# Optimization experiments

Hardware: AMD Instinct MI355X
Metric: run time of the kernel (lower is better)

The kernel has to match this reference:

```python
import jax, jax.numpy as jnp
import numpy as np

N_NODES = 50000
N_EDGES = 800000
HIDDEN = 128
OUT = 128


def setup_inputs() -> dict:
    key = jax.random.key(0)
    k1, k2, k3, k4, k5, k6 = jax.random.split(key, 6)
    h = jax.random.normal(k1, (N_NODES, HIDDEN), dtype=jnp.float32)
    src = jax.random.randint(k2, (N_EDGES,), 0, N_NODES, dtype=jnp.int64)
    dst = jax.random.randint(k3, (N_EDGES,), 0, N_NODES, dtype=jnp.int64)
    scale = 1.0 / np.sqrt(HIDDEN)
    W_edge = jax.random.normal(k4, (OUT, HIDDEN), dtype=jnp.float32) * scale
    W_self = jax.random.normal(k5, (OUT, HIDDEN), dtype=jnp.float32) * scale
    b_self = jax.random.normal(k6, (OUT,), dtype=jnp.float32) * scale
    return {"h": h, "src": src, "dst": dst, "W_edge": W_edge, "W_self": W_self, "b_self": b_self}


def reference(h, src, dst, W_edge, W_self, b_self):
    n = h.shape[0]
    # edge_transform(src_features): same linear on every edge -> transform nodes once, then gather
    msg_node = h @ W_edge.T                       # [N, OUT]
    msg = msg_node[src]                           # [E, OUT] gather
    sums = jax.ops.segment_sum(msg, dst, num_segments=n)  # [N, OUT] scatter-add
    deg = jax.ops.segment_sum(jnp.ones((dst.shape[0],), dtype=h.dtype), dst, num_segments=n)
    h1 = sums / jnp.maximum(deg, 1.0)[:, None]    # mean; zero in-degree -> 0 (DGL semantics)
    out = jax.nn.relu(h @ W_self.T + b_self + h1)
    return out
```

## Files before the change

kernel.cpp:

```cpp
#include <hip/hip_runtime.h>

#define N_HID 128
#define CAP   32
#define OVF_CAP 8192
#define NSLICE 8
#define PBLK   256

typedef short bf16x8 __attribute__((ext_vector_type(8)));
typedef float f32x4  __attribute__((ext_vector_type(4)));

static __device__ __forceinline__ unsigned short f2bf(float f)
{
    unsigned int u = __float_as_uint(f);
    u = (u + 0x7fffu + ((u >> 16) & 1u)) >> 16;
    return (unsigned short)u;
}
static __device__ __forceinline__ unsigned int pack2(float a, float b)
{
    return (unsigned int)f2bf(a) | ((unsigned int)f2bf(b) << 16);
}
static __device__ __forceinline__ float bf2f(unsigned int bits16)
{
    return __uint_as_float(bits16 << 16);
}
static __device__ __forceinline__ int slice_of(int d, float sln)
{
    int sl = (int)((float)d * sln);
    return sl > NSLICE - 1 ? NSLICE - 1 : sl;
}

__global__ __launch_bounds__(256) void count_fragw_cast(
    const int* __restrict__ dst, int* __restrict__ blockCnt,
    int* __restrict__ cnt, int* __restrict__ ovfn, int E, int n, float sln,
    const float* __restrict__ We, const float* __restrict__ Ws,
    unsigned short* __restrict__ Be, unsigned short* __restrict__ Bs,
    const float* __restrict__ h, unsigned short* __restrict__ hbf, int total)
{
    int t = threadIdx.x, b = blockIdx.x;

    if (b >= PBLK + 16) {
        int idx = (b - PBLK - 16) * 2048 + t * 8;
        if (idx + 8 <= total) {
            float4 v0 = *(const float4*)&h[idx];
            float4 v1 = *(const float4*)&h[idx + 4];
            uint4 pk;
            pk.x = pack2(v0.x, v0.y);
            pk.y = pack2(v0.z, v0.w);
            pk.z = pack2(v1.x, v1.y);
            pk.w = pack2(v1.z, v1.w);
            *(uint4*)&hbf[idx] = pk;
        }
        return;
    }

    if (b >= PBLK) {
        int bb = b - PBLK;
        const float* srcw = (bb < 8) ? We : Ws;
        unsigned short* dstF = (bb < 8) ? Be : Bs;
        int rt = bb & 7;
        int kc = t >> 6, l = t & 63, m = l & 15, q = l >> 4;
        const float* p = &srcw[(size_t)(rt * 16 + m) * N_HID + kc * 32 + q * 8];
        float4 v0 = *(const float4*)p;
        float4 v1 = *(const float4*)(p + 4);
        uint4 pk;
        pk.x = pack2(v0.x, v0.y);
        pk.y = pack2(v0.z, v0.w);
        pk.z = pack2(v1.x, v1.y);
        pk.w = pack2(v1.z, v1.w);
        *(uint4*)&dstF[(size_t)rt * 2048 + kc * 512 + l * 8] = pk;
        return;
    }

    for (int i = b * 256 + t; i < n; i += PBLK * 256) cnt[i] = 0;
    if (b == 0 && t == 0) *ovfn = 0;

    int c[NSLICE];
#pragma unroll
    for (int s = 0; s < NSLICE; ++s) c[s] = 0;

    for (int e = b * 256 + t; e < E; e += PBLK * 256) {
        int sl = slice_of(dst[e], sln);
#pragma unroll
        for (int s = 0; s < NSLICE; ++s) c[s] += (sl == s);
    }

    __shared__ int red[NSLICE * 4];
    int lane = t & 63, wid = t >> 6;
#pragma unroll
    for (int s = 0; s < NSLICE; ++s) {
        int v = c[s];
#pragma unroll
        for (int off = 32; off; off >>= 1) v += __shfl_down(v, off);
        if (lane == 0) red[s * 4 + wid] = v;
    }
    __syncthreads();
    if (t < NSLICE)
        blockCnt[t * PBLK + b] = red[t*4+0] + red[t*4+1] + red[t*4+2] + red[t*4+3];
}

__global__ __launch_bounds__(256) void part_scan(
    const int* __restrict__ blockCnt, int* __restrict__ blockBase,
    int* __restrict__ sbase, int E)
{
    __shared__ int wsm[4];
    int t = threadIdx.x, lane = t & 63, wid = t >> 6;
    int v[8]; int s = 0;
#pragma unroll
    for (int i = 0; i < 8; ++i) { v[i] = blockCnt[t * 8 + i]; s += v[i]; }
    int val = s;
#pragma unroll
    for (int off = 1; off < 64; off <<= 1) {
        int y = __shfl_up(val, off);
        if (lane >= off) val += y;
    }
    if (lane == 63) wsm[wid] = val;
    __syncthreads();
    if (t == 0) { int a = 0; for (int w = 0; w < 4; ++w) { int tmp = wsm[w]; wsm[w] = a; a += tmp; } }
    __syncthreads();
    int excl = wsm[wid] + val - s;
#pragma unroll
    for (int i = 0; i < 8; ++i) { int tv = v[i]; blockBase[t * 8 + i] = excl; excl += tv; }
    __syncthreads();
    if (t < NSLICE) sbase[t] = blockBase[t * PBLK];
    if (t == 0)     sbase[NSLICE] = E;
}

__global__ __launch_bounds__(256) void part_scatter(
    const int* __restrict__ src, const int* __restrict__ dst,
    const int* __restrict__ blockBase, unsigned int* __restrict__ part,
    int E, int n, float sln)
{
    __shared__ int cur[NSLICE];
    int t = threadIdx.x, b = blockIdx.x;
    if (t < NSLICE) cur[t] = blockBase[t * PBLK + b];
    __syncthreads();
    for (int e = b * 256 + t; e < E; e += PBLK * 256) {
        int d = dst[e], s = src[e];
        int sl  = slice_of(d, sln);
        int pos = atomicAdd(&cur[sl], 1);
        part[pos] = ((unsigned int)d << 16) | (unsigned int)s;
    }
}

__global__ __launch_bounds__(256) void bucket_scatter2(
    const unsigned int* __restrict__ part,
    const int* __restrict__ sbase,
    int* __restrict__ cnt,
    unsigned short* __restrict__ bucket,
    int* __restrict__ ovfn,
    long long* __restrict__ ovf)
{
    const int slice = blockIdx.x & 7;
    const int g     = blockIdx.x >> 3;
    const int nG    = (int)(gridDim.x >> 3);
    const int lo    = sbase[slice];
    const int hi    = sbase[slice + 1];
    const int m     = hi - lo;

    const int chunk = (m + nG - 1) / nG;
    const int e0 = lo + g * chunk;
    int e1 = e0 + chunk; if (e1 > hi) e1 = hi;

    for (int e = e0 + (int)threadIdx.x; e < e1; e += 256) {
        unsigned int pk = part[e];
        int d = (int)(pk >> 16);
        int s = (int)(pk & 0xffffu);
        int c = atomicAdd(&cnt[d], 1);
        if (c < CAP) {
            bucket[(size_t)d * CAP + c] = (unsigned short)s;
        } else {
            int o = atomicAdd(ovfn, 1);
            if (o < OVF_CAP) ovf[o] = ((long long)d << 32) | (unsigned int)s;
        }
    }
}

__global__ __launch_bounds__(256) void gather_gemm(
    const int* __restrict__ cnt,
    const unsigned short* __restrict__ bucket,
    const int* __restrict__ ovfn,
    const long long* __restrict__ ovf,
    const unsigned short* __restrict__ hbf,
    const unsigned short* __restrict__ Be,
    const unsigned short* __restrict__ Bsf,
    const float* __restrict__ bias,
    float* __restrict__ out,
    int n, int nrt)
{
    __shared__ __align__(16) unsigned int wl[16 * 68];

    const int t    = threadIdx.x;
    const int wid  = t >> 6;
    const int lane = t & 63;
    const int q    = lane >> 4;
    const int s    = lane & 15;
    const int slice = blockIdx.x & 7;
    const int g     = blockIdx.x >> 3;
    const int tLo = (int)(((long long)slice * nrt) >> 3);
    const int tHi = (int)(((long long)(slice + 1) * nrt) >> 3);
    const int tile = tLo + g;
    if (tile >= tHi) return;

    const uint4* h4 = (const uint4*)hbf;
    const unsigned int* h32 = (const unsigned int*)hbf;

    const int nodeBase = tile * 16 + wid * 4;
    int cntv = cnt[tile * 16 + s];
    unsigned int bkv = ((const unsigned int*)bucket)[(size_t)nodeBase * 16 + lane];

#pragma unroll
    for (int k = 0; k < 4; ++k) {
        const int mm   = wid * 4 + k;
        const int node = tile * 16 + mm;
        float a0=0.f,a1=0.f,a2=0.f,a3=0.f,a4=0.f,a5=0.f,a6=0.f,a7=0.f;
        int deg = 0;
        if (node < n) {
            deg = __shfl(cntv, mm);
            int m = deg < CAP ? deg : CAP;
            const int kb = k * 16;

            for (int base = 0; base < m; base += 16) {
                uint4 vr[4]; unsigned int vm[4];
#pragma unroll
                for (int i = 0; i < 4; ++i) {
                    int idx = base + i * 4 + q;
                    int c   = idx < m ? idx : m - 1;
                    unsigned int wsel = (unsigned int)__shfl((int)bkv, kb + (c >> 1));
                    unsigned int r    = (c & 1) ? (wsel >> 16) : (wsel & 0xffffu);
                    vr[i] = h4[(size_t)r * 16 + s];
                    vm[i] = (idx < m) ? 0xffffffffu : 0u;
                }
#pragma unroll
                for (int i = 0; i < 4; ++i) {
                    unsigned int x;
                    x = vr[i].x & vm[i]; a0 += bf2f(x & 0xffffu); a1 += bf2f(x >> 16);
                    x = vr[i].y & vm[i]; a2 += bf2f(x & 0xffffu); a3 += bf2f(x >> 16);
                    x = vr[i].z & vm[i]; a4 += bf2f(x & 0xffffu); a5 += bf2f(x >> 16);
                    x = vr[i].w & vm[i]; a6 += bf2f(x & 0xffffu); a7 += bf2f(x >> 16);
                }
            }

            if (deg > CAP) {
                int no = *ovfn; if (no > OVF_CAP) no = OVF_CAP;
                unsigned int qm = (q == 0) ? 0xffffffffu : 0u;
                for (int o = 0; o < no; ++o) {
                    long long pk = ovf[o];
                    if ((int)(pk >> 32) == node) {
                        uint4 v = h4[(size_t)(unsigned int)pk * 16 + s];
                        unsigned int x;
                        x = v.x & qm; a0 += bf2f(x & 0xffffu); a1 += bf2f(x >> 16);
                        x = v.y & qm; a2 += bf2f(x & 0xffffu); a3 += bf2f(x >> 16);
                        x = v.z & qm; a4 += bf2f(x & 0xffffu); a5 += bf2f(x >> 16);
                        x = v.w & qm; a6 += bf2f(x & 0xffffu); a7 += bf2f(x >> 16);
                    }
                }
            }
        }

#pragma unroll
        for (int off = 16; off <= 32; off <<= 1) {
            a0 += __shfl_xor(a0, off); a1 += __shfl_xor(a1, off);
            a2 += __shfl_xor(a2, off); a3 += __shfl_xor(a3, off);
            a4 += __shfl_xor(a4, off); a5 += __shfl_xor(a5, off);
            a6 += __shfl_xor(a6, off); a7 += __shfl_xor(a7, off);
        }

        float sc = deg > 0 ? 1.0f / (float)deg : 0.f;
        if (q == 0) {
            uint4 pk;
            pk.x = pack2(a0 * sc, a1 * sc);
            pk.y = pack2(a2 * sc, a3 * sc);
            pk.z = pack2(a4 * sc, a5 * sc);
            pk.w = pack2(a6 * sc, a7 * sc);
            *(uint4*)&wl[mm * 68 + 4 * s] = pk;
        }
    }
    __syncthreads();

    const int rr = lane & 15, qq = lane >> 4;
    const int row0 = tile * 16;

    bf16x8 ah[4], ag[4];
#pragma unroll
    for (int kc = 0; kc < 4; ++kc) {
        int gr = row0 + rr; if (gr > n - 1) gr = n - 1;
        ah[kc] = *(const bf16x8*)&hbf[(size_t)gr * N_HID + kc * 32 + qq * 8];
        ag[kc] = *(const bf16x8*)&wl[rr * 68 + kc * 16 + qq * 4];
    }

    const int colb = lane & 15;
    const int rq   = (lane >> 4) * 4;

#pragma unroll
    for (int cti = 0; cti < 2; ++cti) {
        int ct = wid * 2 + cti;
        const bf16x8* BpS = (const bf16x8*)(Bsf + (size_t)ct * 2048);
        const bf16x8* BpE = (const bf16x8*)(Be  + (size_t)ct * 2048);
        f32x4 acc = {0.f, 0.f, 0.f, 0.f};
        acc = __builtin_amdgcn_mfma_f32_16x16x32_bf16(ah[0], BpS[lane],       acc, 0, 0, 0);
        acc = __builtin_amdgcn_mfma_f32_16x16x32_bf16(ah[1], BpS[64 + lane],  acc, 0, 0, 0);
        acc = __builtin_amdgcn_mfma_f32_16x16x32_bf16(ah[2], BpS[128 + lane], acc, 0, 0, 0);
        acc = __builtin_amdgcn_mfma_f32_16x16x32_bf16(ah[3], BpS[192 + lane], acc, 0, 0, 0);
        acc = __builtin_amdgcn_mfma_f32_16x16x32_bf16(ag[0], BpE[lane],       acc, 0, 0, 0);
        acc = __builtin_amdgcn_mfma_f32_16x16x32_bf16(ag[1], BpE[64 + lane],  acc, 0, 0, 0);
        acc = __builtin_amdgcn_mfma_f32_16x16x32_bf16(ag[2], BpE[128 + lane], acc, 0, 0, 0);
        acc = __builtin_amdgcn_mfma_f32_16x16x32_bf16(ag[3], BpE[192 + lane], acc, 0, 0, 0);

        int col = ct * 16 + colb;
        float bv = bias[col];
#pragma unroll
        for (int r = 0; r < 4; ++r) {
            int row = row0 + rq + r;
            if (row < n) out[(size_t)row * N_HID + col] = fmaxf(acc[r] + bv, 0.f);
        }
    }
}

extern "C" void kernel_launch(void* const* d_in, const int* in_sizes, int n_in,
                              void* d_out, int out_size, void* d_ws, size_t ws_size,
                              hipStream_t stream)
{
    const float* h   = (const float*)d_in[0];
    const int*   src = (const int*)d_in[1];
    const int*   dst = (const int*)d_in[2];
    const float* We  = (const float*)d_in[3];
    const float* Ws  = (const float*)d_in[4];
    const float* bs  = (const float*)d_in[5];
    float*       out = (float*)d_out;

    const int n   = in_sizes[0] / N_HID;
    const int E   = in_sizes[1];
    const int nrt = (n + 15) / 16;
    const float sln = (float)NSLICE / (float)n;
    const int total = n * N_HID;

    unsigned short* hbf  = (unsigned short*)d_ws;
    unsigned short* bucket = hbf + (size_t)n * N_HID;
    unsigned short* Be  = bucket + (size_t)n * CAP;
    unsigned short* Bs  = Be + 8 * 2048;
    int*  cnt  = (int*)(Bs + 8 * 2048);
    int*  ovfn = cnt + n;
    long long* ovf = (long long*)(ovfn + 8);
    int*  blockCnt  = (int*)(ovf + OVF_CAP);
    int*  blockBase = blockCnt + PBLK * NSLICE;
    int*  sbase     = blockBase + PBLK * NSLICE;
    unsigned int* part = (unsigned int*)(sbase + 16);

    const int castBlocks = (total + 2047) / 2048;

    const int maxTilesPerSlice = (nrt + NSLICE - 1) / NSLICE;
    const int ggGrid = NSLICE * maxTilesPerSlice;

    count_fragw_cast<<<PBLK + 16 + castBlocks, 256, 0, stream>>>(
        dst, blockCnt, cnt, ovfn, E, n, sln, We, Ws, Be, Bs, h, hbf, total);
    part_scan<<<1, 256, 0, stream>>>(blockCnt, blockBase, sbase, E);
    part_scatter<<<PBLK, 256, 0, stream>>>(src, dst, blockBase, part, E, n, sln);
    bucket_scatter2<<<1024, 256, 0, stream>>>(part, sbase, cnt, bucket, ovfn, ovf);
    gather_gemm<<<ggGrid, 256, 0, stream>>>(cnt, bucket, ovfn, ovf,
                                            hbf, Be, Bs, bs, out, n, nrt);
}
```

Measured before the change: 174.4 us.

## Use sentinel zero row to drop gather masking and double gather block width

Appends a zero row to the bf16 feature copy and pre-fills the bucket array with a sentinel index pointing at it. The gather can then read bucket slots without bounds masking or lane shuffles, using fixed unrolled batches of 16 and a second batch only when degree exceeds 16. The gather_gemm block grows to 512 threads (8 waves, two nodes per wave, one column tile each in the MFMA stage) to raise parallelism. In exchange, an extra pass writes the sentinel into the whole bucket array each call, and every node reads at least 16 rows even when its degree is low.

After: 179.8 us. 3.1% more time.

```diff
diff --git a/kernel.cpp b/kernel.cpp
--- a/kernel.cpp
+++ b/kernel.cpp
@@ -19,9 +19,13 @@
 {
     return (unsigned int)f2bf(a) | ((unsigned int)f2bf(b) << 16);
 }
-static __device__ __forceinline__ float bf2f(unsigned int bits16)
-{
-    return __uint_as_float(bits16 << 16);
+static __device__ __forceinline__ float lo_f(unsigned int x)
+{
+    return __uint_as_float(x << 16);
+}
+static __device__ __forceinline__ float hi_f(unsigned int x)
+{
+    return __uint_as_float(x & 0xffff0000u);
 }
 static __device__ __forceinline__ int slice_of(int d, float sln)
 {
@@ -34,7 +38,8 @@
     int* __restrict__ cnt, int* __restrict__ ovfn, int E, int n, float sln,
     const float* __restrict__ We, const float* __restrict__ Ws,
     unsigned short* __restrict__ Be, unsigned short* __restrict__ Bs,
-    const float* __restrict__ h, unsigned short* __restrict__ hbf, int total)
+    const float* __restrict__ h, unsigned short* __restrict__ hbf, int total,
+    unsigned int* __restrict__ bucket32, unsigned int sent2)
 {
     int t = threadIdx.x, b = blockIdx.x;
 
@@ -49,6 +54,9 @@
             pk.z = pack2(v1.x, v1.y);
             pk.w = pack2(v1.z, v1.w);
             *(uint4*)&hbf[idx] = pk;
+        } else if (idx + 8 <= total + N_HID) {
+            uint4 z = {0u, 0u, 0u, 0u};
+            *(uint4*)&hbf[idx] = z;
         }
         return;
     }
@@ -72,6 +80,10 @@
     }
 
     for (int i = b * 256 + t; i < n; i += PBLK * 256) cnt[i] = 0;
+    {
+        const int nb32 = n * (CAP / 2);
+        for (int i = b * 256 + t; i < nb32; i += PBLK * 256) bucket32[i] = sent2;
+    }
     if (b == 0 && t == 0) *ovfn = 0;
 
     int c[NSLICE];
@@ -175,7 +187,7 @@
     }
 }
 
-__global__ __launch_bounds__(256) void gather_gemm(
+__global__ __launch_bounds__(512) void gather_gemm(
     const int* __restrict__ cnt,
     const unsigned short* __restrict__ bucket,
     const int* __restrict__ ovfn,
@@ -202,57 +214,58 @@
     if (tile >= tHi) return;
 
     const uint4* h4 = (const uint4*)hbf;
-    const unsigned int* h32 = (const unsigned int*)hbf;
-
-    const int nodeBase = tile * 16 + wid * 4;
-    int cntv = cnt[tile * 16 + s];
-    unsigned int bkv = ((const unsigned int*)bucket)[(size_t)nodeBase * 16 + lane];
-
-#pragma unroll
-    for (int k = 0; k < 4; ++k) {
-        const int mm   = wid * 4 + k;
+
+#pragma unroll
+    for (int k = 0; k < 2; ++k) {
+        const int mm   = wid * 2 + k;
         const int node = tile * 16 + mm;
+        const unsigned short* bk = &bucket[(size_t)node * CAP];
         float a0=0.f,a1=0.f,a2=0.f,a3=0.f,a4=0.f,a5=0.f,a6=0.f,a7=0.f;
-        int deg = 0;
-        if (node < n) {
-            deg = __shfl(cntv, mm);
-            int m = deg < CAP ? deg : CAP;
-            const int kb = k * 16;
-
-            for (int base = 0; base < m; base += 16) {
-                uint4 vr[4]; unsigned int vm[4];
-#pragma unroll
-                for (int i = 0; i < 4; ++i) {
-                    int idx = base + i * 4 + q;
-                    int c   = idx < m ? idx : m - 1;
-                    unsigned int wsel = (unsigned int)__shfl((int)bkv, kb + (c >> 1));
-                    unsigned int r    = (c & 1) ? (wsel >> 16) : (wsel & 0xffffu);
-                    vr[i] = h4[(size_t)r * 16 + s];
-                    vm[i] = (idx < m) ? 0xffffffffu : 0u;
-                }
-#pragma unroll
-                for (int i = 0; i < 4; ++i) {
+        int deg = node < n ? cnt[node] : 0;
+
+        {
+            uint4 vr[4];
+#pragma unroll
+            for (int i = 0; i < 4; ++i) {
+                int r = bk[i * 4 + q];
+                vr[i] = h4[(size_t)r * 16 + s];
+            }
+#pragma unroll
+            for (int i = 0; i < 4; ++i) {
+                a0 += lo_f(vr[i].x); a1 += hi_f(vr[i].x);
+                a2 += lo_f(vr[i].y); a3 += hi_f(vr[i].y);
+                a4 += lo_f(vr[i].z); a5 += hi_f(vr[i].z);
+                a6 += lo_f(vr[i].w); a7 += hi_f(vr[i].w);
+            }
+        }
+        if (deg > 16) {
+            uint4 vr[4];
+#pragma unroll
+            for (int i = 0; i < 4; ++i) {
+                int r = bk[16 + i * 4 + q];
+                vr[i] = h4[(size_t)r * 16 + s];
+            }
+#pragma unroll
+            for (int i = 0; i < 4; ++i) {
+                a0 += lo_f(vr[i].x); a1 += hi_f(vr[i].x);
+                a2 += lo_f(vr[i].y); a3 += hi_f(vr[i].y);
+                a4 += lo_f(vr[i].z); a5 += hi_f(vr[i].z);
+                a6 += lo_f(vr[i].w); a7 += hi_f(vr[i].w);
+            }
+        }
+
+        if (deg > CAP) {
+            int no = *ovfn; if (no > OVF_CAP) no = OVF_CAP;
+            unsigned int qm = (q == 0) ? 0xffffffffu : 0u;
+            for (int o = 0; o < no; ++o) {
+                long long pk = ovf[o];
+                if ((int)(pk >> 32) == node) {
+                    uint4 v = h4[(size_t)(unsigned int)pk * 16 + s];
                     unsigned int x;
-                    x = vr[i].x & vm[i]; a0 += bf2f(x & 0xffffu); a1 += bf2f(x >> 16);
-                    x = vr[i].y & vm[i]; a2 += bf2f(x & 0xffffu); a3 += bf2f(x >> 16);
-                    x = vr[i].z & vm[i]; a4 += bf2f(x & 0xffffu); a5 += bf2f(x >> 16);
-                    x = vr[i].w & vm[i]; a6 += bf2f(x & 0xffffu); a7 += bf2f(x >> 16);
-                }
-            }
-
-            if (deg > CAP) {
-                int no = *ovfn; if (no > OVF_CAP) no = OVF_CAP;
-                unsigned int qm = (q == 0) ? 0xffffffffu : 0u;
-                for (int o = 0; o < no; ++o) {
-                    long long pk = ovf[o];
-                    if ((int)(pk >> 32) == node) {
-                        uint4 v = h4[(size_t)(unsigned int)pk * 16 + s];
-                        unsigned int x;
-                        x = v.x & qm; a0 += bf2f(x & 0xffffu); a1 += bf2f(x >> 16);
-                        x = v.y & qm; a2 += bf2f(x & 0xffffu); a3 += bf2f(x >> 16);
-                        x = v.z & qm; a4 += bf2f(x & 0xffffu); a5 += bf2f(x >> 16);
-                        x = v.w & qm; a6 += bf2f(x & 0xffffu); a7 += bf2f(x >> 16);
-                    }
+                    x = v.x & qm; a0 += lo_f(x); a1 += hi_f(x);
+                    x = v.y & qm; a2 += lo_f(x); a3 += hi_f(x);
+                    x = v.z & qm; a4 += lo_f(x); a5 += hi_f(x);
+                    x = v.w & qm; a6 += lo_f(x); a7 += hi_f(x);
                 }
             }
         }
@@ -291,9 +304,8 @@
     const int colb = lane & 15;
     const int rq   = (lane >> 4) * 4;
 
-#pragma unroll
-    for (int cti = 0; cti < 2; ++cti) {
-        int ct = wid * 2 + cti;
+    {
+        int ct = wid;
         const bf16x8* BpS = (const bf16x8*)(Bsf + (size_t)ct * 2048);
         const bf16x8* BpE = (const bf16x8*)(Be  + (size_t)ct * 2048);
         f32x4 acc = {0.f, 0.f, 0.f, 0.f};
@@ -335,7 +347,7 @@
     const int total = n * N_HID;
 
     unsigned short* hbf  = (unsigned short*)d_ws;
-    unsigned short* bucket = hbf + (size_t)n * N_HID;
+    unsigned short* bucket = hbf + (size_t)(n + 1) * N_HID;
     unsigned short* Be  = bucket + (size_t)n * CAP;
     unsigned short* Bs  = Be + 8 * 2048;
     int*  cnt  = (int*)(Bs + 8 * 2048);
@@ -346,16 +358,18 @@
     int*  sbase     = blockBase + PBLK * NSLICE;
     unsigned int* part = (unsigned int*)(sbase + 16);
 
-    const int castBlocks = (total + 2047) / 2048;
+    const unsigned int sent2 = (unsigned int)n | ((unsigned int)n << 16);
+    const int castBlocks = (total + N_HID + 2047) / 2048;
 
     const int maxTilesPerSlice = (nrt + NSLICE - 1) / NSLICE;
     const int ggGrid = NSLICE * maxTilesPerSlice;
 
     count_fragw_cast<<<PBLK + 16 + castBlocks, 256, 0, stream>>>(
-        dst, blockCnt, cnt, ovfn, E, n, sln, We, Ws, Be, Bs, h, hbf, total);
+        dst, blockCnt, cnt, ovfn, E, n, sln, We, Ws, Be, Bs, h, hbf, total,
+        (unsigned int*)bucket, sent2);
     part_scan<<<1, 256, 0, stream>>>(blockCnt, blockBase, sbase, E);
     part_scatter<<<PBLK, 256, 0, stream>>>(src, dst, blockBase, part, E, n, sln);
     bucket_scatter2<<<1024, 256, 0, stream>>>(part, sbase, cnt, bucket, ovfn, ovf);
-    gather_gemm<<<ggGrid, 256, 0, stream>>>(cnt, bucket, ovfn, ovf,
+    gather_gemm<<<ggGrid, 512, 0, stream>>>(cnt, bucket, ovfn, ovf,
                                             hbf, Be, Bs, bs, out, n, nrt);
 }
```
